# Performance work log

Measured on AMD Instinct MI355X. Metric: run time of the kernel, lower is better.

The kernel has to match this reference:

```python
import jax, jax.numpy as jnp
import numpy as np

H = 4096
N_HEADS = 32
N_KV = 8
HEAD_DIM = H // N_HEADS  # 128
GROUPS = N_HEADS // N_KV  # 4
FFN = 11008
EPS = 1e-5
B = 16
S_CACHE = 4096


def _rms(x, w):
    var = jnp.mean(x * x, axis=-1, keepdims=True)
    return w * (x * jax.lax.rsqrt(var + EPS))


def setup_inputs() -> dict:
    key = jax.random.key(0)
    ks = jax.random.split(key, 12)
    s = 0.02
    return {
        "hidden_states": jax.random.normal(ks[0], (B, 1, H), jnp.float32),
        "k_cache": jax.random.normal(ks[1], (B, N_KV, S_CACHE, HEAD_DIM), jnp.float32),
        "v_cache": jax.random.normal(ks[2], (B, N_KV, S_CACHE, HEAD_DIM), jnp.float32),
        "Wq": jax.random.normal(ks[3], (N_HEADS * HEAD_DIM, H), jnp.float32) * s,
        "Wk": jax.random.normal(ks[4], (N_KV * HEAD_DIM, H), jnp.float32) * s,
        "Wv": jax.random.normal(ks[5], (N_KV * HEAD_DIM, H), jnp.float32) * s,
        "Wo": jax.random.normal(ks[6], (H, N_HEADS * HEAD_DIM), jnp.float32) * s,
        "Wg": jax.random.normal(ks[7], (FFN, H), jnp.float32) * s,
        "Wu": jax.random.normal(ks[8], (FFN, H), jnp.float32) * s,
        "Wd": jax.random.normal(ks[9], (H, FFN), jnp.float32) * s,
        "ln1_w": jnp.ones((H,), jnp.float32),
        "ln2_w": jnp.ones((H,), jnp.float32),
    }


def reference(hidden_states, k_cache, v_cache, Wq, Wk, Wv, Wo, Wg, Wu, Wd, ln1_w, ln2_w):
    b = hidden_states.shape[0]
    residual = hidden_states
    h = _rms(hidden_states, ln1_w)  # [B,1,H]

    q = (h @ Wq.T).reshape(b, N_KV, GROUPS, HEAD_DIM)       # [B,kvH,G,D]
    k_new = (h @ Wk.T).reshape(b, N_KV, 1, HEAD_DIM)         # [B,kvH,1,D]
    v_new = (h @ Wv.T).reshape(b, N_KV, 1, HEAD_DIM)

    k = jnp.concatenate([k_cache, k_new], axis=2)            # [B,kvH,S+1,D]
    v = jnp.concatenate([v_cache, v_new], axis=2)

    scale = 1.0 / np.sqrt(HEAD_DIM)
    # GQA without materializing repeated KV heads (same math as repeat_interleave)
    scores = jnp.einsum("bkgd,bksd->bkgs", q, k) * scale      # [B,kvH,G,S+1]
    probs = jax.nn.softmax(scores.astype(jnp.float32), axis=-1).astype(q.dtype)
    attn = jnp.einsum("bkgs,bksd->bkgd", probs, v)            # [B,kvH,G,D]
    attn = attn.reshape(b, 1, N_HEADS * HEAD_DIM)

    h = residual + attn @ Wo.T                                # [B,1,H]

    residual = h
    h = _rms(h, ln2_w)
    mlp = (jax.nn.silu(h @ Wg.T) * (h @ Wu.T)) @ Wd.T
    return residual + mlp
```

## Files before the change

kernel.cpp:

```cpp
#include <hip/hip_runtime.h>
#include <math.h>

#define HH   4096
#define NKV  8
#define GRP  4
#define HD   128
#define FFN  11008
#define NB   16
#define SC   4096
#define SCALE 0.08838834764831845f
#define GTH  1024
#define SCH  512

typedef float f4v __attribute__((ext_vector_type(4)));

__device__ __forceinline__ f4v ntload4(const float* p) {
  return __builtin_nontemporal_load((const f4v*)p);
}
__device__ __forceinline__ float dot4(f4v a, f4v b) {
  return a[0] * b[0] + a[1] * b[1] + a[2] * b[2] + a[3] * b[3];
}

__global__ void rmsnorm_k(const float* __restrict__ x, const float* __restrict__ w,
                          float* __restrict__ y) {
  int b = blockIdx.x;
  const float* xb = x + (size_t)b * HH;
  float* yb = y + (size_t)b * HH;
  int t = threadIdx.x;
  int lane = t & 63, wave = t >> 6;
  f4v v[4];
  float ss = 0.f;
#pragma unroll
  for (int i = 0; i < 4; ++i) {
    v[i] = *(const f4v*)(xb + 4 * (t + 256 * i));
    ss += dot4(v[i], v[i]);
  }
#pragma unroll
  for (int m = 1; m < 64; m <<= 1) ss += __shfl_xor(ss, m);
  __shared__ float red[4];
  if (lane == 0) red[wave] = ss;
  __syncthreads();
  float tot = red[0] + red[1] + red[2] + red[3];
  float rs = rsqrtf(tot * (1.0f / HH) + 1e-5f);
#pragma unroll
  for (int i = 0; i < 4; ++i) {
    int h = 4 * (t + 256 * i);
    f4v wv = *(const f4v*)(w + h);
    f4v o = v[i] * rs * wv;
    *(f4v*)(yb + h) = o;
  }
}

template <int MODE, int WOUT>
__global__ __launch_bounds__(256, 2) void gemv_k(
    const float* __restrict__ W0, const float* __restrict__ W1,
    const float* __restrict__ W2, const float* __restrict__ x0,
    const float* __restrict__ res,
    float* __restrict__ y0, float* __restrict__ y1, float* __restrict__ y2,
    int H) {
  __shared__ float xs[NB * GTH];
  int t = threadIdx.x, lane = t & 63, wave = t >> 6;

  const float* wrow[WOUT];
  int obase;
  if (MODE == 2) {
    int pbase = blockIdx.x * 8 + wave * 2;
    obase = pbase;
    wrow[0] = W0 + (size_t)pbase * H;
    wrow[1] = W1 + (size_t)pbase * H;
    wrow[2] = W0 + (size_t)(pbase + 1) * H;
    wrow[3] = W1 + (size_t)(pbase + 1) * H;
  } else {
    obase = blockIdx.x * (4 * WOUT) + wave * WOUT;
#pragma unroll
    for (int oi = 0; oi < WOUT; ++oi) {
      int o = obase + oi;
      const float* wp;
      if (MODE == 0) {
        if (o < 4096) wp = W0 + (size_t)o * H;
        else if (o < 5120) wp = W1 + (size_t)(o - 4096) * H;
        else wp = W2 + (size_t)(o - 5120) * H;
      } else {
        wp = W0 + (size_t)o * H;
      }
      wrow[oi] = wp;
    }
  }

  float acc[WOUT][NB];
#pragma unroll
  for (int oi = 0; oi < WOUT; ++oi)
#pragma unroll
    for (int b = 0; b < NB; ++b) acc[oi][b] = 0.f;

  for (int hb = 0; hb < H; hb += GTH) {
    int len = H - hb; if (len > GTH) len = GTH;
#pragma unroll
    for (int b = 0; b < NB; ++b) {
      for (int hh = 4 * t; hh < len; hh += 1024) {
        *(f4v*)&xs[b * GTH + hh] = *(const f4v*)(x0 + (size_t)b * H + hb + hh);
      }
    }
    __syncthreads();
    for (int hs = 0; hs < len; hs += 256) {
      int h = hs + 4 * lane;
      f4v w4[WOUT];
#pragma unroll
      for (int oi = 0; oi < WOUT; ++oi) w4[oi] = ntload4(wrow[oi] + hb + h);
#pragma unroll
      for (int b = 0; b < NB; ++b) {
        f4v xv = *(const f4v*)&xs[b * GTH + h];
#pragma unroll
        for (int oi = 0; oi < WOUT; ++oi) acc[oi][b] += dot4(w4[oi], xv);
      }
    }
    __syncthreads();
  }

#define RED(w_, b_, l_) xs[(((w_) * NB + (b_)) * 68) + (l_)]
  float sarr[WOUT];
#pragma unroll
  for (int oi = 0; oi < WOUT; ++oi) {
    asm volatile("s_waitcnt lgkmcnt(0)" ::: "memory");
#pragma unroll
    for (int b = 0; b < NB; ++b) RED(wave, b, lane) = acc[oi][b];
    asm volatile("s_waitcnt lgkmcnt(0)" ::: "memory");
    int rb = lane & 15, rj = lane >> 4;
    const float* rp = &RED(wave, rb, rj * 16);
    f4v a0 = *(const f4v*)rp;
    f4v a1 = *(const f4v*)(rp + 4);
    f4v a2 = *(const f4v*)(rp + 8);
    f4v a3 = *(const f4v*)(rp + 12);
    float s = ((a0[0] + a0[1]) + (a0[2] + a0[3])) + ((a1[0] + a1[1]) + (a1[2] + a1[3])) +
              ((a2[0] + a2[1]) + (a2[2] + a2[3])) + ((a3[0] + a3[1]) + (a3[2] + a3[3]));
    s += __shfl_xor(s, 16);
    s += __shfl_xor(s, 32);
    sarr[oi] = s;
  }
  if (lane < 16) {
    int b = lane;
    if (MODE == 2) {
#pragma unroll
      for (int p = 0; p < 2; ++p) {
        float g = sarr[2 * p], u = sarr[2 * p + 1];
        y0[(size_t)b * FFN + (obase + p)] = g / (1.f + __expf(-g)) * u;
      }
    } else {
#pragma unroll
      for (int oi = 0; oi < WOUT; ++oi) {
        float s = sarr[oi];
        int o = obase + oi;
        if (MODE == 0) {
          if (o < 4096) y0[(size_t)b * 4096 + o] = s;
          else if (o < 5120) y1[(size_t)b * 1024 + (o - 4096)] = s;
          else y2[(size_t)b * 1024 + (o - 5120)] = s;
        } else {
          y0[(size_t)b * 4096 + o] = res[(size_t)b * 4096 + o] + s;
        }
      }
    }
  }
#undef RED
}

__global__ __launch_bounds__(256, 4) void attn_part_k(
    const float* __restrict__ q, const float* __restrict__ kc,
    const float* __restrict__ vc, float* __restrict__ pm,
    float* __restrict__ pl, float* __restrict__ pacc) {
  int c = blockIdx.x, kv = blockIdx.y, b = blockIdx.z;
  int t = threadIdx.x, lane = t & 63, wave = t >> 6;
  int ds = lane & 15, ss = lane >> 4;
  __shared__ float sc[GRP][SCH];
  __shared__ float mg[GRP];
  __shared__ float accw[4][GRP][HD];
  __shared__ float lw[4][GRP];

  f4v qv[GRP][2];
  const float* qb = q + (size_t)b * HH + (size_t)kv * GRP * HD;
#pragma unroll
  for (int g = 0; g < GRP; ++g) {
    qv[g][0] = *(const f4v*)(qb + g * HD + 8 * ds);
    qv[g][1] = *(const f4v*)(qb + g * HD + 8 * ds + 4);
  }
  const size_t kvoff = ((size_t)b * NKV + kv) * (size_t)SC * HD;
  const float* kb = kc + kvoff;

  for (int st = 0; st < SCH / 16; ++st) {
    int sl = st * 16 + wave * 4 + ss;
    const float* kr = kb + (size_t)(c * SCH + sl) * HD + 8 * ds;
    f4v k0 = ntload4(kr);
    f4v k1 = ntload4(kr + 4);
    float d[GRP];
#pragma unroll
    for (int g = 0; g < GRP; ++g)
      d[g] = dot4(qv[g][0], k0) + dot4(qv[g][1], k1);
#pragma unroll
    for (int m = 1; m < 16; m <<= 1)
#pragma unroll
      for (int g = 0; g < GRP; ++g) d[g] += __shfl_xor(d[g], m);
    if (ds < GRP) sc[ds][sl] = d[ds] * SCALE;
  }
  __syncthreads();

  {
    int g = wave;
    float m = -1e30f;
    for (int i = lane; i < SCH; i += 64) m = fmaxf(m, sc[g][i]);
#pragma unroll
    for (int mm = 1; mm < 64; mm <<= 1) m = fmaxf(m, __shfl_xor(m, mm));
    if (lane == 0) mg[g] = m;
  }
  __syncthreads();
  float mreg[GRP];
#pragma unroll
  for (int g = 0; g < GRP; ++g) mreg[g] = mg[g];

  float acc[GRP][8];
  float lacc[GRP];
#pragma unroll
  for (int g = 0; g < GRP; ++g) {
    lacc[g] = 0.f;
#pragma unroll
    for (int j = 0; j < 8; ++j) acc[g][j] = 0.f;
  }
  const float* vb = vc + kvoff;
  for (int st = 0; st < SCH / 16; ++st) {
    int sl = st * 16 + wave * 4 + ss;
    const float* vr = vb + (size_t)(c * SCH + sl) * HD + 8 * ds;
    f4v v0 = ntload4(vr);
    f4v v1 = ntload4(vr + 4);
    float p[GRP];
#pragma unroll
    for (int g = 0; g < GRP; ++g) p[g] = __expf(sc[g][sl] - mreg[g]);
    if (ds == 0) {
#pragma unroll
      for (int g = 0; g < GRP; ++g) lacc[g] += p[g];
    }
#pragma unroll
    for (int g = 0; g < GRP; ++g) {
#pragma unroll
      for (int j = 0; j < 4; ++j) {
        acc[g][j] += p[g] * v0[j];
        acc[g][4 + j] += p[g] * v1[j];
      }
    }
  }
#pragma unroll
  for (int m = 16; m < 64; m <<= 1) {
#pragma unroll
    for (int g = 0; g < GRP; ++g) {
#pragma unroll
      for (int j = 0; j < 8; ++j) acc[g][j] += __shfl_xor(acc[g][j], m);
      lacc[g] += __shfl_xor(lacc[g], m);
    }
  }
  if (ss == 0) {
#pragma unroll
    for (int g = 0; g < GRP; ++g) {
#pragma unroll
      for (int j = 0; j < 4; ++j) {
        accw[wave][g][8 * ds + j] = acc[g][j];
        accw[wave][g][8 * ds + 4 + j] = acc[g][4 + j];
      }
    }
    if (ds == 0) {
#pragma unroll
      for (int g = 0; g < GRP; ++g) lw[wave][g] = lacc[g];
    }
  }
  __syncthreads();

  size_t pbase = (((size_t)(b * NKV + kv)) * 8 + c) * GRP;
  for (int idx = t; idx < GRP * HD; idx += 256) {
    int g = idx >> 7, dd = idx & 127;
    float o = accw[0][g][dd] + accw[1][g][dd] + accw[2][g][dd] + accw[3][g][dd];
    pacc[(pbase + g) * HD + dd] = o;
  }
  if (t < GRP) {
    pm[pbase + t] = mg[t];
    pl[pbase + t] = lw[0][t] + lw[1][t] + lw[2][t] + lw[3][t];
  }
}

__global__ void attn_red_k(const float* __restrict__ q, const float* __restrict__ knew,
                           const float* __restrict__ vnew, const float* __restrict__ pm,
                           const float* __restrict__ pl, const float* __restrict__ pacc,
                           float* __restrict__ attn) {
  int bi = blockIdx.x;
  int b = bi >> 3, kv = bi & 7;
  int t = threadIdx.x, lane = t & 63, wave = t >> 6;
  __shared__ float sn[GRP];
  {
    int g = wave;
    float2 qv = *(const float2*)(q + (size_t)b * HH + (size_t)(kv * GRP + g) * HD + 2 * lane);
    float2 k2 = *(const float2*)(knew + (size_t)b * (NKV * HD) + kv * HD + 2 * lane);
    float d = qv.x * k2.x + qv.y * k2.y;
#pragma unroll
    for (int m = 1; m < 64; m <<= 1) d += __shfl_xor(d, m);
    if (lane == 0) sn[g] = d * SCALE;
  }
  __syncthreads();
  size_t base = ((size_t)(b * NKV + kv)) * 8;
  for (int idx = t; idx < GRP * HD; idx += 256) {
    int g = idx >> 7, dd = idx & 127;
    float snv = sn[g];
    float M = snv;
    float pmv[8];
#pragma unroll
    for (int cc = 0; cc < 8; ++cc) {
      pmv[cc] = pm[(base + cc) * GRP + g];
      M = fmaxf(M, pmv[cc]);
    }
    float en = __expf(snv - M);
    float L = en;
    float o = en * vnew[(size_t)b * (NKV * HD) + kv * HD + dd];
#pragma unroll
    for (int cc = 0; cc < 8; ++cc) {
      float f = __expf(pmv[cc] - M);
      L += f * pl[(base + cc) * GRP + g];
      o += f * pacc[((base + cc) * GRP + g) * HD + dd];
    }
    attn[(size_t)b * HH + (size_t)(kv * GRP + g) * HD + dd] = o / L;
  }
}

extern "C" void kernel_launch(void* const* d_in, const int* in_sizes, int n_in,
                              void* d_out, int out_size, void* d_ws, size_t ws_size,
                              hipStream_t stream) {
  const float* hidden = (const float*)d_in[0];
  const float* kc = (const float*)d_in[1];
  const float* vc = (const float*)d_in[2];
  const float* Wq = (const float*)d_in[3];
  const float* Wk = (const float*)d_in[4];
  const float* Wv = (const float*)d_in[5];
  const float* Wo = (const float*)d_in[6];
  const float* Wg = (const float*)d_in[7];
  const float* Wu = (const float*)d_in[8];
  const float* Wd = (const float*)d_in[9];
  const float* ln1 = (const float*)d_in[10];
  const float* ln2 = (const float*)d_in[11];
  float* out = (float*)d_out;

  float* ws = (float*)d_ws;
  float* xn1 = ws;
  float* qb = xn1 + 65536;
  float* kn = qb + 65536;
  float* vn = kn + 16384;
  float* attn = vn + 16384;
  float* h2 = attn + 65536;
  float* xn2 = h2 + 65536;
  float* gu = xn2 + 65536;
  float* pm = gu + 176128;
  float* pl = pm + 4096;
  float* pacc = pl + 4096;

  rmsnorm_k<<<16, 256, 0, stream>>>(hidden, ln1, xn1);
  gemv_k<0, 2><<<768, 256, 0, stream>>>(Wq, Wk, Wv, xn1, nullptr,
                                        qb, kn, vn, 4096);
  attn_part_k<<<dim3(8, 8, 16), 256, 0, stream>>>(qb, kc, vc, pm, pl, pacc);
  attn_red_k<<<128, 256, 0, stream>>>(qb, kn, vn, pm, pl, pacc, attn);
  gemv_k<1, 2><<<512, 256, 0, stream>>>(Wo, nullptr, nullptr, attn, hidden,
                                        h2, nullptr, nullptr, 4096);
  rmsnorm_k<<<16, 256, 0, stream>>>(h2, ln2, xn2);
  gemv_k<2, 4><<<1376, 256, 0, stream>>>(Wg, Wu, nullptr, xn2, nullptr,
                                         gu, nullptr, nullptr, 4096);
  gemv_k<3, 2><<<512, 256, 0, stream>>>(Wd, nullptr, nullptr, gu, h2,
                                        out, nullptr, nullptr, 11008);
}
```

Baseline: 295.2 us.

## Drop LDS staging of activations in GEMV, read x directly from cache

The GEMV kernel no longer copies the 16 activation vectors into shared memory in 1024-wide chunks with block barriers. Each lane now reads activations straight from global memory, relying on L1/L2 hits. Blocks shrink to 128 threads and every wave handles 4 output rows, which frees LDS for higher occupancy and removes the __syncthreads. The trade-off is more global/L1 traffic for the activations and higher register pressure from 64 accumulators.

After: 474.0 us. 1.61x slower.

```diff
diff --git a/kernel.cpp b/kernel.cpp
--- a/kernel.cpp
+++ b/kernel.cpp
@@ -9,7 +9,6 @@
 #define NB   16
 #define SC   4096
 #define SCALE 0.08838834764831845f
-#define GTH  1024
 #define SCH  512
 
 typedef float f4v __attribute__((ext_vector_type(4)));
@@ -51,29 +50,28 @@
   }
 }
 
-template <int MODE, int WOUT>
-__global__ __launch_bounds__(256, 2) void gemv_k(
+template <int MODE>
+__global__ __launch_bounds__(128, 2) void gemv_k(
     const float* __restrict__ W0, const float* __restrict__ W1,
     const float* __restrict__ W2, const float* __restrict__ x0,
     const float* __restrict__ res,
     float* __restrict__ y0, float* __restrict__ y1, float* __restrict__ y2,
     int H) {
-  __shared__ float xs[NB * GTH];
   int t = threadIdx.x, lane = t & 63, wave = t >> 6;
 
-  const float* wrow[WOUT];
+  const float* wrow[4];
   int obase;
   if (MODE == 2) {
-    int pbase = blockIdx.x * 8 + wave * 2;
+    int pbase = blockIdx.x * 4 + wave * 2;
     obase = pbase;
     wrow[0] = W0 + (size_t)pbase * H;
     wrow[1] = W1 + (size_t)pbase * H;
     wrow[2] = W0 + (size_t)(pbase + 1) * H;
     wrow[3] = W1 + (size_t)(pbase + 1) * H;
   } else {
-    obase = blockIdx.x * (4 * WOUT) + wave * WOUT;
-#pragma unroll
-    for (int oi = 0; oi < WOUT; ++oi) {
+    obase = blockIdx.x * 8 + wave * 4;
+#pragma unroll
+    for (int oi = 0; oi < 4; ++oi) {
       int o = obase + oi;
       const float* wp;
       if (MODE == 0) {
@@ -87,46 +85,39 @@
     }
   }
 
-  float acc[WOUT][NB];
-#pragma unroll
-  for (int oi = 0; oi < WOUT; ++oi)
+  const float* xp[NB];
+#pragma unroll
+  for (int b = 0; b < NB; ++b) xp[b] = x0 + (size_t)b * H;
+
+  float acc[4][NB];
+#pragma unroll
+  for (int oi = 0; oi < 4; ++oi)
 #pragma unroll
     for (int b = 0; b < NB; ++b) acc[oi][b] = 0.f;
 
-  for (int hb = 0; hb < H; hb += GTH) {
-    int len = H - hb; if (len > GTH) len = GTH;
+#pragma unroll 2
+  for (int h = 4 * lane; h < H; h += 256) {
+    f4v w4[4];
+#pragma unroll
+    for (int oi = 0; oi < 4; ++oi) w4[oi] = ntload4(wrow[oi] + h);
 #pragma unroll
     for (int b = 0; b < NB; ++b) {
-      for (int hh = 4 * t; hh < len; hh += 1024) {
-        *(f4v*)&xs[b * GTH + hh] = *(const f4v*)(x0 + (size_t)b * H + hb + hh);
-      }
-    }
-    __syncthreads();
-    for (int hs = 0; hs < len; hs += 256) {
-      int h = hs + 4 * lane;
-      f4v w4[WOUT];
-#pragma unroll
-      for (int oi = 0; oi < WOUT; ++oi) w4[oi] = ntload4(wrow[oi] + hb + h);
-#pragma unroll
-      for (int b = 0; b < NB; ++b) {
-        f4v xv = *(const f4v*)&xs[b * GTH + h];
-#pragma unroll
-        for (int oi = 0; oi < WOUT; ++oi) acc[oi][b] += dot4(w4[oi], xv);
-      }
-    }
-    __syncthreads();
-  }
-
-#define RED(w_, b_, l_) xs[(((w_) * NB + (b_)) * 68) + (l_)]
-  float sarr[WOUT];
-#pragma unroll
-  for (int oi = 0; oi < WOUT; ++oi) {
+      f4v xv = *(const f4v*)(xp[b] + h);
+#pragma unroll
+      for (int oi = 0; oi < 4; ++oi) acc[oi][b] += dot4(w4[oi], xv);
+    }
+  }
+
+  __shared__ float red[2][NB][68];
+  float sarr[4];
+#pragma unroll
+  for (int oi = 0; oi < 4; ++oi) {
     asm volatile("s_waitcnt lgkmcnt(0)" ::: "memory");
 #pragma unroll
-    for (int b = 0; b < NB; ++b) RED(wave, b, lane) = acc[oi][b];
+    for (int b = 0; b < NB; ++b) red[wave][b][lane] = acc[oi][b];
     asm volatile("s_waitcnt lgkmcnt(0)" ::: "memory");
     int rb = lane & 15, rj = lane >> 4;
-    const float* rp = &RED(wave, rb, rj * 16);
+    const float* rp = &red[wave][rb][rj * 16];
     f4v a0 = *(const f4v*)rp;
     f4v a1 = *(const f4v*)(rp + 4);
     f4v a2 = *(const f4v*)(rp + 8);
@@ -147,7 +138,7 @@
       }
     } else {
 #pragma unroll
-      for (int oi = 0; oi < WOUT; ++oi) {
+      for (int oi = 0; oi < 4; ++oi) {
         float s = sarr[oi];
         int o = obase + oi;
         if (MODE == 0) {
@@ -160,7 +151,6 @@
       }
     }
   }
-#undef RED
 }
 
 __global__ __launch_bounds__(256, 4) void attn_part_k(
@@ -355,15 +345,15 @@
   float* pacc = pl + 4096;
 
   rmsnorm_k<<<16, 256, 0, stream>>>(hidden, ln1, xn1);
-  gemv_k<0, 2><<<768, 256, 0, stream>>>(Wq, Wk, Wv, xn1, nullptr,
-                                        qb, kn, vn, 4096);
+  gemv_k<0><<<768, 128, 0, stream>>>(Wq, Wk, Wv, xn1, nullptr,
+                                     qb, kn, vn, 4096);
   attn_part_k<<<dim3(8, 8, 16), 256, 0, stream>>>(qb, kc, vc, pm, pl, pacc);
   attn_red_k<<<128, 256, 0, stream>>>(qb, kn, vn, pm, pl, pacc, attn);
-  gemv_k<1, 2><<<512, 256, 0, stream>>>(Wo, nullptr, nullptr, attn, hidden,
-                                        h2, nullptr, nullptr, 4096);
+  gemv_k<1><<<512, 128, 0, stream>>>(Wo, nullptr, nullptr, attn, hidden,
+                                     h2, nullptr, nullptr, 4096);
   rmsnorm_k<<<16, 256, 0, stream>>>(h2, ln2, xn2);
-  gemv_k<2, 4><<<1376, 256, 0, stream>>>(Wg, Wu, nullptr, xn2, nullptr,
-                                         gu, nullptr, nullptr, 4096);
-  gemv_k<3, 2><<<512, 256, 0, stream>>>(Wd, nullptr, nullptr, gu, h2,
-                                        out, nullptr, nullptr, 11008);
-}
+  gemv_k<2><<<2752, 128, 0, stream>>>(Wg, Wu, nullptr, xn2, nullptr,
+                                      gu, nullptr, nullptr, 4096);
+  gemv_k<3><<<512, 128, 0, stream>>>(Wd, nullptr, nullptr, gu, h2,
+                                     out, nullptr, nullptr, 11008);
+}
```
